# Kernel optimization log

Hardware: AMD Instinct MI355X
Metric: run time of the kernel (lower is better)

Reference implementation:

```python
import jax, jax.numpy as jnp
import numpy as np

B, L, E, H, K = 256, 500, 300, 10, 5  # batch, doc_len, word_embedding, h1, num_aspects


def setup_inputs() -> dict:
    key = jax.random.key(0)
    k1, k2, k3 = jax.random.split(key, 3)
    review = jax.random.normal(k1, (B, L, E), dtype=jnp.float32)
    # params initialized uniform(-0.01, 0.01) as in the torch module
    aspProj = jax.random.uniform(k2, (K, E, H), dtype=jnp.float32, minval=-0.01, maxval=0.01)
    aspEmbed = jax.random.uniform(k3, (K, 3 * H), dtype=jnp.float32, minval=-0.01, maxval=0.01)
    return {"review": review, "aspProj": aspProj, "aspEmbed": aspEmbed}


def reference(review, aspProj, aspEmbed):
    # project review into each aspect subspace: (K, B, L, H)
    proj = jnp.einsum('ble,keh->kblh', review, aspProj)
    # pad seq dim by 1 on each side, build window-3 unfold.
    # torch unfold(1,3,1) yields (B, L, H, 3) then reshape to (B, L, 3*H),
    # i.e. feature layout is (h_index, window_offset) -- match by stacking
    # window offsets on the LAST axis before the reshape.
    padded = jnp.pad(proj, ((0, 0), (0, 0), (1, 1), (0, 0)))
    windows = jnp.stack([padded[:, :, i:i + L, :] for i in range(3)], axis=-1)  # (K,B,L,H,3)
    windows = windows.reshape(K, windows.shape[1], L, 3 * H)  # (K,B,L,3H)
    # attention logits per position, softmax over the WHOLE sequence dim
    scores = jnp.einsum('kblf,kf->kbl', windows, aspEmbed)
    attn = jax.nn.softmax(scores, axis=-1)  # (K,B,L)
    # attention-weighted sum over sequence -> aspect representation
    rep = jnp.einsum('kblh,kbl->kbh', proj, attn)  # (K,B,H)
    batch_aspAttn = jnp.transpose(attn, (1, 0, 2))  # (B,K,L)
    batch_aspRep = jnp.transpose(rep, (1, 0, 2))    # (B,K,H)
    return (batch_aspAttn, batch_aspRep)
```

## Files before the change

kernel.cpp:

```cpp
#include <hip/hip_runtime.h>

#define BB 256
#define LL 500
#define EE 300
#define HH 10
#define KK 5
#define NF 50
#define NT 512
#define NWAVE 8

#define MP 512
#define CK 32
#define NCH 10
#define AP 40
#define BP 328
#define PP 53
#define NR4 75
#define NA4 3750

#define B_OFF    (2 * MP * AP * 2)
#define B_BYTES  (64 * BP * 2)
#define SD_OFF   (MP * PP * 4)
#define RED_OFF  (SD_OFF + 3 * KK * MP * 4)
#define REP_OFF  (RED_OFF + KK * NWAVE * 4)
#define EMB_OFF  (REP_OFF + NWAVE * NF * 4)
#define SMEM_BYTES (EMB_OFF + KK * 3 * HH * 4)

typedef __attribute__((ext_vector_type(8))) short short8;
typedef __attribute__((ext_vector_type(4))) float f32x4;

__device__ __forceinline__ unsigned int f2bf(float x) {
    unsigned int u = __float_as_uint(x);
    return (u + 0x7FFFu + ((u >> 16) & 1u)) >> 16;
}

__global__ __launch_bounds__(NT, 2) void anr_mfma3(
    const float* __restrict__ review,
    const float* __restrict__ aspProj,
    const float* __restrict__ aspEmbed,
    float* __restrict__ out)
{
    __shared__ __align__(16) char smem[SMEM_BYTES];
    short* B16   = (short*)(smem + B_OFF);
    float* proj  = (float*)smem;
    float* s_d   = (float*)(smem + SD_OFF);
    float* s_red = (float*)(smem + RED_OFF);
    float* s_rep = (float*)(smem + REP_OFF);
    float* s_emb = (float*)(smem + EMB_OFF);

    const int tid  = threadIdx.x;
    const int b    = blockIdx.x;
    const int lane = tid & 63;
    const int w    = tid >> 6;
    const int quad = lane >> 4;
    const int m16  = lane & 15;
    const int q    = tid & 7;
    const int r0   = tid >> 3;

    for (int j = tid; j < B_BYTES / 4; j += NT)
        ((int*)(smem + B_OFF))[j] = 0;
    __syncthreads();

    const float4* rev4 = (const float4*)review + (size_t)b * LL * NR4;
    const float4* rp[8];
#pragma unroll
    for (int i = 0; i < 8; ++i) {
        int r = r0 + 64 * i;
        rp[i] = rev4 + (size_t)((r < LL) ? r : (LL - 1)) * NR4;
    }

    const float4* ap4 = (const float4*)aspProj;
    float4 bt[8];
#pragma unroll
    for (int i = 0; i < 8; ++i) {
        int idx = tid + NT * i;
        bt[i] = ap4[(idx < NA4) ? idx : (NA4 - 1)];
    }
    float embv = aspEmbed[(tid < KK * 3 * HH) ? tid : 0];
    float4 ld[8];
#pragma unroll
    for (int i = 0; i < 8; ++i) ld[i] = rp[i][q];

#pragma unroll
    for (int i = 0; i < 8; ++i) {
        int idx = tid + NT * i;
        if (idx < NA4) {
            float vv[4] = {bt[i].x, bt[i].y, bt[i].z, bt[i].w};
#pragma unroll
            for (int cm = 0; cm < 4; ++cm) {
                int jj   = 4 * idx + cm;
                int kasp = jj / (EE * HH);
                int rr   = jj - kasp * (EE * HH);
                int e    = rr / HH;
                int h    = rr - e * HH;
                B16[(kasp * HH + h) * BP + e] = (short)f2bf(vv[cm]);
            }
        }
    }
    if (tid < KK * 3 * HH) s_emb[tid] = embv;

    {
        short* An = (short*)smem;
#pragma unroll
        for (int i = 0; i < 8; ++i) {
            int r = r0 + 64 * i;
            uint2 pk;
            pk.x = f2bf(ld[i].x) | (f2bf(ld[i].y) << 16);
            pk.y = f2bf(ld[i].z) | (f2bf(ld[i].w) << 16);
            *(uint2*)&An[r * AP + q * 4] = pk;
        }
    }
    __syncthreads();

    f32x4 acc[4][4];
#pragma unroll
    for (int mi = 0; mi < 4; ++mi)
#pragma unroll
        for (int ni = 0; ni < 4; ++ni)
            acc[mi][ni] = (f32x4){0.f, 0.f, 0.f, 0.f};

#pragma unroll
    for (int c = 0; c < NCH; ++c) {
        if (c + 1 < NCH) {
            int fq = 8 * (c + 1) + q;
            if (fq > NR4 - 1) fq = NR4 - 1;
#pragma unroll
            for (int i = 0; i < 8; ++i) ld[i] = rp[i][fq];
        }
        const short* Ac = (const short*)smem + (c & 1) * (MP * AP);
        short8 af[4], bf[4];
#pragma unroll
        for (int mi = 0; mi < 4; ++mi)
            af[mi] = *(const short8*)&Ac[(w * 64 + mi * 16 + m16) * AP + quad * 8];
#pragma unroll
        for (int ni = 0; ni < 4; ++ni)
            bf[ni] = *(const short8*)&B16[(ni * 16 + m16) * BP + c * CK + quad * 8];
#pragma unroll
        for (int mi = 0; mi < 4; ++mi)
#pragma unroll
            for (int ni = 0; ni < 4; ++ni)
                acc[mi][ni] = __builtin_amdgcn_mfma_f32_16x16x32_bf16(
                    af[mi], bf[ni], acc[mi][ni], 0, 0, 0);
        if (c + 1 < NCH) {
            short* An = (short*)smem + ((c + 1) & 1) * (MP * AP);
#pragma unroll
            for (int i = 0; i < 8; ++i) {
                int r = r0 + 64 * i;
                uint2 pk;
                pk.x = f2bf(ld[i].x) | (f2bf(ld[i].y) << 16);
                pk.y = f2bf(ld[i].z) | (f2bf(ld[i].w) << 16);
                *(uint2*)&An[r * AP + q * 4] = pk;
            }
            __syncthreads();
        }
    }

    __syncthreads();
#pragma unroll
    for (int mi = 0; mi < 4; ++mi) {
#pragma unroll
        for (int ni = 0; ni < 4; ++ni) {
            int col = ni * 16 + m16;
            if (col < NF) {
                int row = w * 64 + mi * 16 + quad * 4;
#pragma unroll
                for (int r = 0; r < 4; ++r)
                    proj[(row + r) * PP + col] = acc[mi][ni][r];
            }
        }
    }
    __syncthreads();

    const int l  = tid;
    const bool vl = (l < LL);

    float pr[NF];
#pragma unroll
    for (int f = 0; f < NF; ++f) pr[f] = proj[l * PP + f];

    float d0[KK], d1[KK], d2[KK];
#pragma unroll
    for (int k = 0; k < KK; ++k) {
        float a0 = 0.f, a1 = 0.f, a2 = 0.f;
#pragma unroll
        for (int h = 0; h < HH; ++h) {
            float x = pr[k * HH + h];
            a0 = fmaf(x, s_emb[k * 3 * HH + 3 * h + 0], a0);
            a1 = fmaf(x, s_emb[k * 3 * HH + 3 * h + 1], a1);
            a2 = fmaf(x, s_emb[k * 3 * HH + 3 * h + 2], a2);
        }
        d0[k] = vl ? a0 : 0.f;
        d1[k] = vl ? a1 : 0.f;
        d2[k] = vl ? a2 : 0.f;
    }
#pragma unroll
    for (int k = 0; k < KK; ++k) {
        s_d[(0 * KK + k) * MP + l] = d0[k];
        s_d[(1 * KK + k) * MP + l] = d1[k];
        s_d[(2 * KK + k) * MP + l] = d2[k];
    }
    __syncthreads();

    const int lp1 = (l + 1 < MP) ? l + 1 : MP - 1;
    float sc[KK];
#pragma unroll
    for (int k = 0; k < KK; ++k) {
        float t0 = (l >= 1) ? s_d[(0 * KK + k) * MP + l - 1] : 0.f;
        float t1 = s_d[(1 * KK + k) * MP + l];
        float t2 = s_d[(2 * KK + k) * MP + lp1];
        sc[k] = vl ? (t0 + t1 + t2) : -1e30f;
    }

    float mx[KK];
#pragma unroll
    for (int k = 0; k < KK; ++k) {
        float m = sc[k];
        for (int s = 32; s > 0; s >>= 1) m = fmaxf(m, __shfl_xor(m, s, 64));
        if (lane == 0) s_red[k * NWAVE + w] = m;
    }
    __syncthreads();
#pragma unroll
    for (int k = 0; k < KK; ++k) {
        float m = s_red[k * NWAVE + 0];
#pragma unroll
        for (int ww = 1; ww < NWAVE; ++ww) m = fmaxf(m, s_red[k * NWAVE + ww]);
        mx[k] = m;
    }
    __syncthreads();
    float ex[KK], sm[KK];
#pragma unroll
    for (int k = 0; k < KK; ++k) {
        ex[k] = __expf(sc[k] - mx[k]);
        float s = ex[k];
        for (int sh = 32; sh > 0; sh >>= 1) s += __shfl_xor(s, sh, 64);
        if (lane == 0) s_red[k * NWAVE + w] = s;
    }
    __syncthreads();
#pragma unroll
    for (int k = 0; k < KK; ++k) {
        float s = 0.f;
#pragma unroll
        for (int ww = 0; ww < NWAVE; ++ww) s += s_red[k * NWAVE + ww];
        sm[k] = s;
    }

#pragma unroll
    for (int k = 0; k < KK; ++k) {
        float wk = ex[k] / sm[k];
        if (vl) out[((size_t)b * KK + k) * LL + l] = wk;
#pragma unroll
        for (int h = 0; h < HH; ++h) {
            float v = pr[k * HH + h] * wk;
            for (int sh = 32; sh > 0; sh >>= 1) v += __shfl_xor(v, sh, 64);
            if (lane == 0) s_rep[w * NF + k * HH + h] = v;
        }
    }
    __syncthreads();
    if (tid < NF) {
        float s = 0.f;
#pragma unroll
        for (int ww = 0; ww < NWAVE; ++ww) s += s_rep[ww * NF + tid];
        out[(size_t)BB * KK * LL + (size_t)b * NF + tid] = s;
    }
}

extern "C" void kernel_launch(void* const* d_in, const int* in_sizes, int n_in,
                              void* d_out, int out_size, void* d_ws, size_t ws_size,
                              hipStream_t stream) {
    const float* review   = (const float*)d_in[0];
    const float* aspProj  = (const float*)d_in[1];
    const float* aspEmbed = (const float*)d_in[2];
    float* out = (float*)d_out;

    anr_mfma3<<<dim3(BB), dim3(NT), 0, stream>>>(review, aspProj, aspEmbed, out);
}
```

Baseline: 238.7 us.

## Feed MFMA A-fragments straight from global memory, dropping LDS staging

Each lane now loads its review-row A-fragment from global memory in MFMA layout, converts it to bf16 in registers, and prefetches the next chunk into registers. This removes the double-buffered LDS A tiles and the barrier after every K chunk. The last chunk is zero-masked at the E boundary, and the window-term scratch now reuses the B buffer region, which shrinks LDS. The cost is more live registers and global reads of 32 bytes per lane that are less cooperative than the old layout.

Result: no change. 239.8 us (+0.5%).

```diff
diff --git a/kernel.cpp b/kernel.cpp
--- a/kernel.cpp
+++ b/kernel.cpp
@@ -12,16 +12,13 @@
 #define MP 512
 #define CK 32
 #define NCH 10
-#define AP 40
 #define BP 328
 #define PP 53
-#define NR4 75
 #define NA4 3750
 
-#define B_OFF    (2 * MP * AP * 2)
 #define B_BYTES  (64 * BP * 2)
-#define SD_OFF   (MP * PP * 4)
-#define RED_OFF  (SD_OFF + 3 * KK * MP * 4)
+#define PROJ_OFF B_BYTES
+#define RED_OFF  (PROJ_OFF + MP * PP * 4)
 #define REP_OFF  (RED_OFF + KK * NWAVE * 4)
 #define EMB_OFF  (REP_OFF + NWAVE * NF * 4)
 #define SMEM_BYTES (EMB_OFF + KK * 3 * HH * 4)
@@ -34,16 +31,25 @@
     return (u + 0x7FFFu + ((u >> 16) & 1u)) >> 16;
 }
 
-__global__ __launch_bounds__(NT, 2) void anr_mfma3(
+__device__ __forceinline__ short8 pack8(float4 a, float4 b) {
+    short8 r;
+    r[0] = (short)f2bf(a.x); r[1] = (short)f2bf(a.y);
+    r[2] = (short)f2bf(a.z); r[3] = (short)f2bf(a.w);
+    r[4] = (short)f2bf(b.x); r[5] = (short)f2bf(b.y);
+    r[6] = (short)f2bf(b.z); r[7] = (short)f2bf(b.w);
+    return r;
+}
+
+__global__ __launch_bounds__(NT, 2) void anr_mfma4(
     const float* __restrict__ review,
     const float* __restrict__ aspProj,
     const float* __restrict__ aspEmbed,
     float* __restrict__ out)
 {
     __shared__ __align__(16) char smem[SMEM_BYTES];
-    short* B16   = (short*)(smem + B_OFF);
-    float* proj  = (float*)smem;
-    float* s_d   = (float*)(smem + SD_OFF);
+    short* B16   = (short*)smem;
+    float* s_d   = (float*)smem;
+    float* proj  = (float*)(smem + PROJ_OFF);
     float* s_red = (float*)(smem + RED_OFF);
     float* s_rep = (float*)(smem + REP_OFF);
     float* s_emb = (float*)(smem + EMB_OFF);
@@ -54,20 +60,9 @@
     const int w    = tid >> 6;
     const int quad = lane >> 4;
     const int m16  = lane & 15;
-    const int q    = tid & 7;
-    const int r0   = tid >> 3;
 
     for (int j = tid; j < B_BYTES / 4; j += NT)
-        ((int*)(smem + B_OFF))[j] = 0;
-    __syncthreads();
-
-    const float4* rev4 = (const float4*)review + (size_t)b * LL * NR4;
-    const float4* rp[8];
-#pragma unroll
-    for (int i = 0; i < 8; ++i) {
-        int r = r0 + 64 * i;
-        rp[i] = rev4 + (size_t)((r < LL) ? r : (LL - 1)) * NR4;
-    }
+        ((int*)smem)[j] = 0;
 
     const float4* ap4 = (const float4*)aspProj;
     float4 bt[8];
@@ -77,9 +72,22 @@
         bt[i] = ap4[(idx < NA4) ? idx : (NA4 - 1)];
     }
     float embv = aspEmbed[(tid < KK * 3 * HH) ? tid : 0];
-    float4 ld[8];
-#pragma unroll
-    for (int i = 0; i < 8; ++i) ld[i] = rp[i][q];
+
+    const float* revb = review + (size_t)b * LL * EE;
+    const float* ar[4];
+#pragma unroll
+    for (int mi = 0; mi < 4; ++mi) {
+        int r = w * 64 + mi * 16 + m16;
+        ar[mi] = revb + (size_t)((r < LL) ? r : (LL - 1)) * EE + quad * 8;
+    }
+    float4 fc[4][2], fn[4][2];
+#pragma unroll
+    for (int mi = 0; mi < 4; ++mi) {
+        fc[mi][0] = *(const float4*)(ar[mi] + 0);
+        fc[mi][1] = *(const float4*)(ar[mi] + 4);
+    }
+
+    __syncthreads();
 
 #pragma unroll
     for (int i = 0; i < 8; ++i) {
@@ -98,18 +106,6 @@
         }
     }
     if (tid < KK * 3 * HH) s_emb[tid] = embv;
-
-    {
-        short* An = (short*)smem;
-#pragma unroll
-        for (int i = 0; i < 8; ++i) {
-            int r = r0 + 64 * i;
-            uint2 pk;
-            pk.x = f2bf(ld[i].x) | (f2bf(ld[i].y) << 16);
-            pk.y = f2bf(ld[i].z) | (f2bf(ld[i].w) << 16);
-            *(uint2*)&An[r * AP + q * 4] = pk;
-        }
-    }
     __syncthreads();
 
     f32x4 acc[4][4];
@@ -120,42 +116,57 @@
             acc[mi][ni] = (f32x4){0.f, 0.f, 0.f, 0.f};
 
 #pragma unroll
-    for (int c = 0; c < NCH; ++c) {
-        if (c + 1 < NCH) {
-            int fq = 8 * (c + 1) + q;
-            if (fq > NR4 - 1) fq = NR4 - 1;
-#pragma unroll
-            for (int i = 0; i < 8; ++i) ld[i] = rp[i][fq];
-        }
-        const short* Ac = (const short*)smem + (c & 1) * (MP * AP);
-        short8 af[4], bf[4];
-#pragma unroll
-        for (int mi = 0; mi < 4; ++mi)
-            af[mi] = *(const short8*)&Ac[(w * 64 + mi * 16 + m16) * AP + quad * 8];
+    for (int c = 0; c < NCH - 1; ++c) {
+        if (c < NCH - 2) {
+#pragma unroll
+            for (int mi = 0; mi < 4; ++mi) {
+                fn[mi][0] = *(const float4*)(ar[mi] + (c + 1) * CK);
+                fn[mi][1] = *(const float4*)(ar[mi] + (c + 1) * CK + 4);
+            }
+        } else {
+            const float4 z4 = {0.f, 0.f, 0.f, 0.f};
+#pragma unroll
+            for (int mi = 0; mi < 4; ++mi) {
+                fn[mi][0] = (quad < 2) ? *(const float4*)(ar[mi] + (NCH - 1) * CK) : z4;
+                fn[mi][1] = (quad < 1) ? *(const float4*)(ar[mi] + (NCH - 1) * CK + 4) : z4;
+            }
+        }
+        short8 bf[4], af[4];
 #pragma unroll
         for (int ni = 0; ni < 4; ++ni)
             bf[ni] = *(const short8*)&B16[(ni * 16 + m16) * BP + c * CK + quad * 8];
+#pragma unroll
+        for (int mi = 0; mi < 4; ++mi)
+            af[mi] = pack8(fc[mi][0], fc[mi][1]);
 #pragma unroll
         for (int mi = 0; mi < 4; ++mi)
 #pragma unroll
             for (int ni = 0; ni < 4; ++ni)
                 acc[mi][ni] = __builtin_amdgcn_mfma_f32_16x16x32_bf16(
                     af[mi], bf[ni], acc[mi][ni], 0, 0, 0);
-        if (c + 1 < NCH) {
-            short* An = (short*)smem + ((c + 1) & 1) * (MP * AP);
-#pragma unroll
-            for (int i = 0; i < 8; ++i) {
-                int r = r0 + 64 * i;
-                uint2 pk;
-                pk.x = f2bf(ld[i].x) | (f2bf(ld[i].y) << 16);
-                pk.y = f2bf(ld[i].z) | (f2bf(ld[i].w) << 16);
-                *(uint2*)&An[r * AP + q * 4] = pk;
-            }
-            __syncthreads();
-        }
-    }
-
-    __syncthreads();
+#pragma unroll
+        for (int mi = 0; mi < 4; ++mi) {
+            fc[mi][0] = fn[mi][0];
+            fc[mi][1] = fn[mi][1];
+        }
+    }
+    {
+        const int c = NCH - 1;
+        short8 bf[4], af[4];
+#pragma unroll
+        for (int ni = 0; ni < 4; ++ni)
+            bf[ni] = *(const short8*)&B16[(ni * 16 + m16) * BP + c * CK + quad * 8];
+#pragma unroll
+        for (int mi = 0; mi < 4; ++mi)
+            af[mi] = pack8(fc[mi][0], fc[mi][1]);
+#pragma unroll
+        for (int mi = 0; mi < 4; ++mi)
+#pragma unroll
+            for (int ni = 0; ni < 4; ++ni)
+                acc[mi][ni] = __builtin_amdgcn_mfma_f32_16x16x32_bf16(
+                    af[mi], bf[ni], acc[mi][ni], 0, 0, 0);
+    }
+
 #pragma unroll
     for (int mi = 0; mi < 4; ++mi) {
 #pragma unroll
@@ -272,5 +283,5 @@
     const float* aspEmbed = (const float*)d_in[2];
     float* out = (float*)d_out;
 
-    anr_mfma3<<<dim3(BB), dim3(NT), 0, stream>>>(review, aspProj, aspEmbed, out);
-}
+    anr_mfma4<<<dim3(BB), dim3(NT), 0, stream>>>(review, aspProj, aspEmbed, out);
+}
```
